# Kernel optimization log

Measured on AMD Instinct MI355X. Metric: run time of the kernel, lower is better.

## Reference

```python
import jax, jax.numpy as jnp
import numpy as np

N, E, C, H = 50000, 250000, 7, 64
D = C + 2  # node feature dim after concatenating labels


def _mlp2(x, w1, b1, w2, b2):
    return jnp.maximum(x @ w1 + b1, 0.0) @ w2 + b2


def _lin(key, fi, fo, bias=True):
    lim = 1.0 / np.sqrt(fi)
    kw, kb = jax.random.split(key)
    w = jax.random.uniform(kw, (fi, fo), jnp.float32, -lim, lim)
    if bias:
        b = jax.random.uniform(kb, (fo,), jnp.float32, -lim, lim)
        return w, b
    return w


def setup_inputs() -> dict:
    key = jax.random.key(0)
    ks = jax.random.split(key, 16)
    v = jax.random.normal(ks[0], (N, C), jnp.float32)
    labels = jnp.zeros((N, 2), jnp.float32).at[0, 1].set(1.0)  # node 0 is the goal
    edge_index = jax.random.randint(ks[1], (2, E), 0, N)
    hx_w1, hx_b1 = _lin(ks[2], 4 * D, H)
    hx_w2, hx_b2 = _lin(ks[3], H, H)
    hy_w1, hy_b1 = _lin(ks[4], 3 * D, H)
    hy_w2, hy_b2 = _lin(ks[5], H, H)
    fx_w1, fx_b1 = _lin(ks[6], 4 * H, H)
    fx_w2, fx_b2 = _lin(ks[7], H, H)
    fy_w1, fy_b1 = _lin(ks[8], 3 * H, H)
    fy_w2, fy_b2 = _lin(ks[9], H, H)
    feta_w1, feta_b1 = _lin(ks[10], H, H)
    feta_w2, feta_b2 = _lin(ks[11], H, H)
    feta_w3 = _lin(ks[12], H, 1, bias=False)
    return dict(v=v, labels=labels, edge_index=edge_index, loop=3,
                hx_w1=hx_w1, hx_b1=hx_b1, hx_w2=hx_w2, hx_b2=hx_b2,
                hy_w1=hy_w1, hy_b1=hy_b1, hy_w2=hy_w2, hy_b2=hy_b2,
                fx_w1=fx_w1, fx_b1=fx_b1, fx_w2=fx_w2, fx_b2=fx_b2,
                fy_w1=fy_w1, fy_b1=fy_b1, fy_w2=fy_w2, fy_b2=fy_b2,
                feta_w1=feta_w1, feta_b1=feta_b1, feta_w2=feta_w2, feta_b2=feta_b2,
                feta_w3=feta_w3)


def reference(v, labels, edge_index, loop,
              hx_w1, hx_b1, hx_w2, hx_b2,
              hy_w1, hy_b1, hy_w2, hy_b2,
              fx_w1, fx_b1, fx_w2, fx_b2,
              fy_w1, fy_b1, fy_w2, fy_b2,
              feta_w1, feta_b1, feta_w2, feta_b2, feta_w3):
    n = v.shape[0]
    vc = jnp.concatenate([v, labels], axis=-1)              # [N, D]
    goal = vc[jnp.argmax(labels[:, 1])][None, :]             # [1, D]
    d = vc - goal
    x = _mlp2(jnp.concatenate([vc, jnp.broadcast_to(goal, vc.shape), d, d * d], -1),
              hx_w1, hx_b1, hx_w2, hx_b2)                    # [N, H]
    src, dst = edge_index[0], edge_index[1]
    vi, vj = vc[src], vc[dst]
    y = _mlp2(jnp.concatenate([vj - vi, vj, vi], -1), hy_w1, hy_b1, hy_w2, hy_b2)  # [E, H]
    for _ in range(loop):
        # MPNN (PyG default flow): x_j = source = edge_index[0], x_i = target = edge_index[1]
        xj_m, xi_m = x[src], x[dst]
        m = _mlp2(jnp.concatenate([xj_m - xi_m, xj_m, xi_m, y], -1),
                  fx_w1, fx_b1, fx_w2, fx_b2)                # [E, H]
        agg = jax.ops.segment_max(m, dst, num_segments=n)    # scatter-max to targets; empty -> -inf
        x = jnp.maximum(x, agg)                              # -inf absorbed by max with x
        xi, xj = x[src], x[dst]                              # Explorer: i=edge_index[0], j=edge_index[1]
        y = jnp.maximum(y, _mlp2(jnp.concatenate([xj - xi, xj, xi], -1),
                                 fy_w1, fy_b1, fy_w2, fy_b2))
    h = jnp.maximum(x @ feta_w1 + feta_b1, 0.0)
    h = jnp.maximum(h @ feta_w2 + feta_b2, 0.0)
    return h @ feta_w3                                       # [N, 1]
```

## Files before the change

kernel.cpp:

```cpp
#include <hip/hip_runtime.h>
#include <math.h>

typedef unsigned short u16;
typedef unsigned int u32;
typedef unsigned long long u64;
typedef __attribute__((ext_vector_type(8))) _Float16 f16x8;
typedef __attribute__((ext_vector_type(2))) _Float16 f16x2;
typedef __attribute__((ext_vector_type(4))) float f32x4;

union U8h { f16x8 v; f16x2 p[4]; u32 u[4]; _Float16 s[8]; };
union U4h { _Float16 s[4]; u64 u; };

__device__ __forceinline__ void atomicMaxF(float* addr, float val) {
  if (val >= 0.0f) {
    atomicMax((int*)addr, __float_as_int(val));
  } else {
    atomicMin((unsigned int*)addr, (unsigned int)__float_as_int(val));
  }
}

__device__ __forceinline__ f16x2 pk(float a, float b) {
  return __builtin_bit_cast(f16x2, __builtin_amdgcn_cvt_pkrtz(a, b));
}

__device__ __forceinline__ void dec8h(const float* f, U8h& h, U8h& l) {
#pragma unroll
  for (int i = 0; i < 4; ++i) {
    float a = f[2 * i], b = f[2 * i + 1];
    f16x2 hp = pk(a, b);
    float ra = a - (float)hp[0];
    float rb = b - (float)hp[1];
    h.p[i] = hp;
    l.p[i] = pk(ra, rb);
  }
}

__device__ __forceinline__ void conv8_rne(const float* f, U8h& h) {
#pragma unroll
  for (int i = 0; i < 8; ++i) h.s[i] = (_Float16)f[i];
}

__device__ __forceinline__ void load_row(const float* p, float* f) {
  *(float4*)(f + 0)  = *(const float4*)(p);
  *(float4*)(f + 4)  = *(const float4*)(p + 4);
  *(float4*)(f + 8)  = *(const float4*)(p + 32);
  *(float4*)(f + 12) = *(const float4*)(p + 36);
}

struct RunCtx { bool chain1, chain2, chain3, suppress; };

__device__ __forceinline__ RunCtx run_ctx(const int dd[4], int lane, int q) {
  bool allsame = (dd[0] == dd[1]) && (dd[1] == dd[2]) && (dd[2] == dd[3]);
  int nfd1 = __shfl(dd[0], lane + 16, 64);
  int nfd2 = __shfl(dd[0], lane + 32, 64);
  int nfd3 = __shfl(dd[0], lane + 48, 64);
  int as = allsame ? 1 : 0;
  int nas1 = __shfl(as, lane + 16, 64);
  int nas2 = __shfl(as, lane + 32, 64);
  int pld = __shfl(dd[3], lane - 16, 64);
  RunCtx c;
  c.chain1 = (q < 3) && (nfd1 == dd[3]);
  c.chain2 = c.chain1 && (nas1 != 0) && (q < 2) && (nfd2 == dd[3]);
  c.chain3 = c.chain2 && (nas2 != 0) && (q < 1) && (nfd3 == dd[3]);
  c.suppress = (q > 0) && (pld == dd[0]);
  return c;
}

__device__ __forceinline__ void emit_t(const f32x4 o, const int dd[4], const RunCtx c,
                                       int lane, int m, int t, float* __restrict__ xnew) {
// ... 150 lines not shown
      for (int k = 0; k < 9; ++k) s += g[k] * hxw1[(9 + k) * 64 + c];
      b1p[c] = s;
    }
    return;
  }
  __shared__ int red[256];
  int s = 0;
  for (int i = threadIdx.x; i < 1024; i += 256) {
    int idx = b * 1024 + i;
    s += (idx < N) ? deg[idx] : 0;
  }
  red[threadIdx.x] = s; __syncthreads();
  for (int st = 128; st > 0; st >>= 1) {
    if (threadIdx.x < st) red[threadIdx.x] += red[threadIdx.x + st];
    __syncthreads();
  }
  if (threadIdx.x == 0) bsum[b] = red[0];
}

__global__ __launch_bounds__(256) void k_hx2s(
    const float* __restrict__ vcp, const float* __restrict__ goal,
    const _Float16* __restrict__ B1, const float* __restrict__ b1p,
    const _Float16* __restrict__ B2, const float* __restrict__ b2,
    float* __restrict__ xout, float* __restrict__ xout2, _Float16* __restrict__ xh, int N,
    const int* __restrict__ deg, const int* __restrict__ bsum, int* __restrict__ cursor, int NB) {
  if ((int)blockIdx.x >= NB) {
    __shared__ int lsum[256];
    __shared__ int bofs;
    int b = blockIdx.x - NB;
    int tid = threadIdx.x;
    if (tid == 0) {
      int a = 0;
      for (int i = 0; i < b; ++i) a += bsum[i];
      bofs = a;
    }
    int base_i = b * 1024 + tid * 4;
    int loc[4]; int s = 0;
#pragma unroll
    for (int j = 0; j < 4; ++j) {
      int vv = (base_i + j < N) ? deg[base_i + j] : 0;
      loc[j] = s; s += vv;
    }
    lsum[tid] = s; __syncthreads();
    for (int st = 1; st < 256; st <<= 1) {
      int add = (tid >= st) ? lsum[tid - st] : 0;
      __syncthreads();
      lsum[tid] += add;
      __syncthreads();
    }
    int toff = bofs + lsum[tid] - s;
#pragma unroll
    for (int j = 0; j < 4; ++j) {
      if (base_i + j < N) cursor[base_i + j] = toff + loc[j];
    }
    return;
  }
  __shared__ float hbuf[4][16 * 68];
  const int lane = threadIdx.x & 63;
  const int wv = threadIdx.x >> 6;
  const int m = lane & 15, q = lane >> 4;
  const int base = blockIdx.x * 64 + wv * 16;
  int node = base + m; if (node >= N) node = N - 1;
  float vc[12];
  *(float4*)(vc + 0) = *(const float4*)(vcp + (size_t)node * 16);
  *(float4*)(vc + 4) = *(const float4*)(vcp + (size_t)node * 16 + 4);
  *(float4*)(vc + 8) = *(const float4*)(vcp + (size_t)node * 16 + 8);
  float gl[9];
#pragma unroll
  for (int i = 0; i < 9; ++i) gl[i] = goal[i];
  float f[8];
#pragma unroll
  for (int j = 0; j < 8; ++j) {
    int idx = q * 8 + j;
    float val = 0.f;
    if (idx < 9) val = vc[idx];
    else if (idx < 18) val = vc[idx - 9] - gl[idx - 9];
    else if (idx < 27) { float dv = vc[idx - 18] - gl[idx - 18]; val = dv * dv; }
    f[j] = val;
  }
  U8h Ah, Al;
  dec8h(f, Ah, Al);

  f32x4 acc[4];
#pragma unroll
  for (int t = 0; t < 4; ++t) { float bv = b1p[t * 16 + m]; acc[t] = (f32x4){bv, bv, bv, bv}; }
#pragma unroll
  for (int t = 0; t < 4; ++t) {
    f16x8 b = *(const f16x8*)(B1 + ((size_t)t * 64 + lane) * 8);
    acc[t] = __builtin_amdgcn_mfma_f32_16x16x32_f16(Ah.v, b, acc[t], 0, 0, 0);
    acc[t] = __builtin_amdgcn_mfma_f32_16x16x32_f16(Al.v, b, acc[t], 0, 0, 0);
  }

  float* hb = hbuf[wv];
#pragma unroll
  for (int t = 0; t < 4; ++t)
#pragma unroll
    for (int r = 0; r < 4; ++r)
      hb[(q * 4 + r) * 68 + t * 16 + m] = fmaxf(acc[t][r], 0.f);

  float fh[16];
  load_row(hb + m * 68 + q * 8, fh);
  U8h A2h[2], A2l[2];
  dec8h(fh + 0, A2h[0], A2l[0]);
  dec8h(fh + 8, A2h[1], A2l[1]);

  f32x4 acc2[4];
#pragma unroll
  for (int t = 0; t < 4; ++t) { float bv = b2[t * 16 + m]; acc2[t] = (f32x4){bv, bv, bv, bv}; }
#pragma unroll
  for (int c = 0; c < 2; ++c) {
#pragma unroll
    for (int t = 0; t < 4; ++t) {
      f16x8 b = *(const f16x8*)(B2 + ((size_t)(c * 4 + t) * 64 + lane) * 8);
      acc2[t] = __builtin_amdgcn_mfma_f32_16x16x32_f16(A2h[c].v, b, acc2[t], 0, 0, 0);
      acc2[t] = __builtin_amdgcn_mfma_f32_16x16x32_f16(A2l[c].v, b, acc2[t], 0, 0, 0);
    }
  }

#pragma unroll
  for (int t = 0; t < 4; ++t)
#pragma unroll
    for (int r = 0; r < 4; ++r)
      hb[(q * 4 + r) * 68 + t * 16 + m] = acc2[t][r];

  int row = base + m;
  if (row < N) {
    float ov[16];
    const float* orow = hb + m * 68 + q * 16;
    *(float4*)(ov + 0)  = *(const float4*)(orow);
    *(float4*)(ov + 4)  = *(const float4*)(orow + 4);
    *(float4*)(ov + 8)  = *(const float4*)(orow + 8);
    *(float4*)(ov + 12) = *(const float4*)(orow + 12);
    float* p1 = xout + (size_t)row * 64 + q * 16;
    float* p2 = xout2 + (size_t)row * 64 + q * 16;
#pragma unroll
    for (int i = 0; i < 4; ++i) {
      *(float4*)(p1 + i * 4) = *(const float4*)(ov + i * 4);
      *(float4*)(p2 + i * 4) = *(const float4*)(ov + i * 4);
    }
    U8h X0, X1;
    conv8_rne(ov + 0, X0);
    conv8_rne(ov + 8, X1);
    *(f16x8*)(xh + (size_t)row * 64 + q * 16)     = X0.v;
    *(f16x8*)(xh + (size_t)row * 64 + q * 16 + 8) = X1.v;
  }
}

__global__ __launch_bounds__(256) void k_scatter(const int* __restrict__ src,
                                                 const int* __restrict__ dst, int E,
                                                 int* __restrict__ cursor,
                                                 int* __restrict__ srcp, int* __restrict__ dstp) {
  int e = blockIdx.x * 256 + threadIdx.x;
  if (e < E) {
    int d = dst[e];
    int pos = atomicAdd(&cursor[d], 1);
    srcp[pos] = src[e];
    dstp[pos] = d;
  }
}

__global__ __launch_bounds__(256) void k_cc(const float4* __restrict__ s,
                                            float4* __restrict__ d,
                                            _Float16* __restrict__ h16, int n4) {
  int i = blockIdx.x * 256 + threadIdx.x;
  if (i < n4) {
    float4 v = s[i];
    d[i] = v;
    U4h o;
    o.s[0] = (_Float16)v.x; o.s[1] = (_Float16)v.y;
    o.s[2] = (_Float16)v.z; o.s[3] = (_Float16)v.w;
    *(u64*)(h16 + (size_t)i * 4) = o.u;
  }
}

__global__ __launch_bounds__(256) void k_hyfx(
    const float* __restrict__ vcp, const _Float16* __restrict__ xh,
    const int* __restrict__ src, const int* __restrict__ dst,
    const _Float16* __restrict__ hB1, const float* __restrict__ hb1,
    const _Float16* __restrict__ hB2, const float* __restrict__ hb2,
    const _Float16* __restrict__ xB1, const float* __restrict__ xb1,
    const _Float16* __restrict__ xB2, const float* __restrict__ xb2,
    _Float16* __restrict__ y, float* __restrict__ xnew, int E) {
  __shared__ float hbuf[4][16 * 68];
  const int lane = threadIdx.x & 63;
  const int wv = threadIdx.x >> 6;
  const int m = lane & 15, q = lane >> 4;
  const int base = blockIdx.x * 64 + wv * 16;
  int em = base + m; if (em >= E) em = E - 1;
  const int si = src[em], di = dst[em];
  const int row = base + m;
  const bool live = row < E;

  int dd[4];
  int e0 = base + q * 4;
#pragma unroll
  for (int r = 0; r < 4; ++r) {
    int e2 = e0 + r;
    dd[r] = (e2 < E) ? dst[e2] : -1;
  }
  const int node = (q < 2) ? di : si;
  const float* p = vcp + (size_t)node * 16 + (q & 1) * 8;
  float f[8];
  *(float4*)(f + 0) = *(const float4*)(p);
  *(float4*)(f + 4) = *(const float4*)(p + 4);
  const _Float16* ps = xh + (size_t)si * 64 + q * 8;
  const _Float16* pd = xh + (size_t)di * 64 + q * 8;
  U8h Xs0, Xs1, Xd0, Xd1;
  Xs0.v = *(const f16x8*)ps;         Xs1.v = *(const f16x8*)(ps + 32);
  Xd0.v = *(const f16x8*)pd;         Xd1.v = *(const f16x8*)(pd + 32);

  U8h Ah, Al;
  dec8h(f, Ah, Al);

  f32x4 acc[4];
#pragma unroll
  for (int t = 0; t < 4; ++t) { float bv = hb1[t * 16 + m]; acc[t] = (f32x4){bv, bv, bv, bv}; }
#pragma unroll
  for (int t = 0; t < 4; ++t) {
    f16x8 b = *(const f16x8*)(hB1 + ((size_t)t * 64 + lane) * 8);
    acc[t] = __builtin_amdgcn_mfma_f32_16x16x32_f16(Ah.v, b, acc[t], 0, 0, 0);
    acc[t] = __builtin_amdgcn_mfma_f32_16x16x32_f16(Al.v, b, acc[t], 0, 0, 0);
  }

  float* hb = hbuf[wv];
#pragma unroll
  for (int t = 0; t < 4; ++t)
#pragma unroll
    for (int r = 0; r < 4; ++r)
      hb[(q * 4 + r) * 68 + t * 16 + m] = fmaxf(acc[t][r], 0.f);

  float fh[16];
  load_row(hb + m * 68 + q * 8, fh);
  U8h H0, H1;
  conv8_rne(fh + 0, H0);
  conv8_rne(fh + 8, H1);

  f32x4 o[4];
#pragma unroll
  for (int t = 0; t < 4; ++t) { float bv = hb2[t * 16 + m]; o[t] = (f32x4){bv, bv, bv, bv}; }
#pragma unroll
  for (int t = 0; t < 4; ++t) {
    f16x8 b0 = *(const f16x8*)(hB2 + ((size_t)(0 * 4 + t) * 64 + lane) * 8);
    f16x8 b1_ = *(const f16x8*)(hB2 + ((size_t)(1 * 4 + t) * 64 + lane) * 8);
    o[t] = __builtin_amdgcn_mfma_f32_16x16x32_f16(H0.v, b0, o[t], 0, 0, 0);
    o[t] = __builtin_amdgcn_mfma_f32_16x16x32_f16(H1.v, b1_, o[t], 0, 0, 0);
  }

#pragma unroll
  for (int t = 0; t < 4; ++t)
#pragma unroll
    for (int r = 0; r < 4; ++r)
      hb[(q * 4 + r) * 68 + t * 16 + m] = o[t][r];

  float nv[16];
  load_row(hb + m * 68 + q * 8, nv);
  U8h Yh0, Yh1;
  conv8_rne(nv + 0, Yh0);
  conv8_rne(nv + 8, Yh1);
  if (live) {
    size_t yo = (size_t)row * 64 + q * 8;
    *(f16x8*)(y + yo)      = Yh0.v;
    *(f16x8*)(y + yo + 32) = Yh1.v;
  }

  f32x4 acc2[4];
#pragma unroll
  for (int t = 0; t < 4; ++t) { float bv = xb1[t * 16 + m]; acc2[t] = (f32x4){bv, bv, bv, bv}; }
#pragma unroll
  for (int t = 0; t < 4; ++t) {
    f16x8 b0 = *(const f16x8*)(xB1 + ((size_t)(0 * 4 + t) * 64 + lane) * 8);
    f16x8 b1_ = *(const f16x8*)(xB1 + ((size_t)(1 * 4 + t) * 64 + lane) * 8);
    f16x8 b2_ = *(const f16x8*)(xB1 + ((size_t)(2 * 4 + t) * 64 + lane) * 8);
    f16x8 b3_ = *(const f16x8*)(xB1 + ((size_t)(3 * 4 + t) * 64 + lane) * 8);
    f16x8 b4_ = *(const f16x8*)(xB1 + ((size_t)(4 * 4 + t) * 64 + lane) * 8);
    f16x8 b5_ = *(const f16x8*)(xB1 + ((size_t)(5 * 4 + t) * 64 + lane) * 8);
    acc2[t] = __builtin_amdgcn_mfma_f32_16x16x32_f16(Xs0.v, b0, acc2[t], 0, 0, 0);
    acc2[t] = __builtin_amdgcn_mfma_f32_16x16x32_f16(Xs1.v, b1_, acc2[t], 0, 0, 0);
    acc2[t] = __builtin_amdgcn_mfma_f32_16x16x32_f16(Xd0.v, b2_, acc2[t], 0, 0, 0);
    acc2[t] = __builtin_amdgcn_mfma_f32_16x16x32_f16(Xd1.v, b3_, acc2[t], 0, 0, 0);
    acc2[t] = __builtin_amdgcn_mfma_f32_16x16x32_f16(Yh0.v, b4_, acc2[t], 0, 0, 0);
    acc2[t] = __builtin_amdgcn_mfma_f32_16x16x32_f16(Yh1.v, b5_, acc2[t], 0, 0, 0);
  }

#pragma unroll
  for (int t = 0; t < 4; ++t)
#pragma unroll
    for (int r = 0; r < 4; ++r)
      hb[(q * 4 + r) * 68 + t * 16 + m] = fmaxf(acc2[t][r], 0.f);

  float fh2[16];
  load_row(hb + m * 68 + q * 8, fh2);
  U8h G0, G1;
  conv8_rne(fh2 + 0, G0);
  conv8_rne(fh2 + 8, G1);

  f32x4 o2[4];
#pragma unroll
  for (int t = 0; t < 4; ++t) { float bv = xb2[t * 16 + m]; o2[t] = (f32x4){bv, bv, bv, bv}; }
#pragma unroll
  for (int t = 0; t < 4; ++t) {
    f16x8 b0 = *(const f16x8*)(xB2 + ((size_t)(0 * 4 + t) * 64 + lane) * 8);
    f16x8 b1_ = *(const f16x8*)(xB2 + ((size_t)(1 * 4 + t) * 64 + lane) * 8);
    o2[t] = __builtin_amdgcn_mfma_f32_16x16x32_f16(G0.v, b0, o2[t], 0, 0, 0);
    o2[t] = __builtin_amdgcn_mfma_f32_16x16x32_f16(G1.v, b1_, o2[t], 0, 0, 0);
  }

  RunCtx rc = run_ctx(dd, lane, q);
#pragma unroll
  for (int t = 0; t < 4; ++t) emit_t(o2[t], dd, rc, lane, m, t, xnew);
}

__global__ __launch_bounds__(256) void k_fyfx(
    const _Float16* __restrict__ xh, _Float16* __restrict__ y,
    const int* __restrict__ src, const int* __restrict__ dst,
    const _Float16* __restrict__ yB1, const float* __restrict__ yb1,
    const _Float16* __restrict__ yB2, const float* __restrict__ yb2,
    const _Float16* __restrict__ xB1, const float* __restrict__ xb1,
    const _Float16* __restrict__ xB2, const float* __restrict__ xb2,
    float* __restrict__ xnew, int E, int storeY) {
  __shared__ float hbuf[8][16 * 68];
  const int lane = threadIdx.x & 63;
  const int wv = threadIdx.x >> 6;
  const int m = lane & 15, q = lane >> 4;
  const int b0e = blockIdx.x * 128 + wv * 16;

  float* hb0 = hbuf[wv];
  float* hb1 = hbuf[4 + wv];

  int em0 = b0e + m;       if (em0 >= E) em0 = E - 1;
  int em1 = b0e + 64 + m;  if (em1 >= E) em1 = E - 1;
  const int si0 = src[em0], di0 = dst[em0];
  const int si1 = src[em1], di1 = dst[em1];
  const bool live0 = (b0e + m) < E;
  const bool live1 = (b0e + 64 + m) < E;

  U8h Xs0[2], Xs1[2], Xd0[2], Xd1[2], Ho0[2], Ho1[2];
  {
    const _Float16* ps = xh + (size_t)si0 * 64 + q * 8;
    const _Float16* pd = xh + (size_t)di0 * 64 + q * 8;
    Xs0[0].v = *(const f16x8*)ps;  Xs1[0].v = *(const f16x8*)(ps + 32);
    Xd0[0].v = *(const f16x8*)pd;  Xd1[0].v = *(const f16x8*)(pd + 32);
  }
  {
    const _Float16* ps = xh + (size_t)si1 * 64 + q * 8;
    const _Float16* pd = xh + (size_t)di1 * 64 + q * 8;
    Xs0[1].v = *(const f16x8*)ps;  Xs1[1].v = *(const f16x8*)(ps + 32);
    Xd0[1].v = *(const f16x8*)pd;  Xd1[1].v = *(const f16x8*)(pd + 32);
  }
  {
    size_t yo0 = (size_t)em0 * 64 + q * 8;
// ... 8 lines not shown
    float bv = yb1[t * 16 + m];
    acc[0][t] = (f32x4){bv, bv, bv, bv};
    acc[1][t] = acc[0][t];
  }
#pragma unroll
  for (int t = 0; t < 4; ++t) {
    f16x8 w0 = *(const f16x8*)(yB1 + ((size_t)(0 * 4 + t) * 64 + lane) * 8);
    f16x8 w1 = *(const f16x8*)(yB1 + ((size_t)(1 * 4 + t) * 64 + lane) * 8);
    f16x8 w2 = *(const f16x8*)(yB1 + ((size_t)(2 * 4 + t) * 64 + lane) * 8);
    f16x8 w3 = *(const f16x8*)(yB1 + ((size_t)(3 * 4 + t) * 64 + lane) * 8);
#pragma unroll
    for (int u = 0; u < 2; ++u) {
      acc[u][t] = __builtin_amdgcn_mfma_f32_16x16x32_f16(Xd0[u].v, w0, acc[u][t], 0, 0, 0);
      acc[u][t] = __builtin_amdgcn_mfma_f32_16x16x32_f16(Xd1[u].v, w1, acc[u][t], 0, 0, 0);
      acc[u][t] = __builtin_amdgcn_mfma_f32_16x16x32_f16(Xs0[u].v, w2, acc[u][t], 0, 0, 0);
      acc[u][t] = __builtin_amdgcn_mfma_f32_16x16x32_f16(Xs1[u].v, w3, acc[u][t], 0, 0, 0);
    }
  }

#pragma unroll
  for (int t = 0; t < 4; ++t)
#pragma unroll
    for (int r = 0; r < 4; ++r) {
      hb0[(q * 4 + r) * 68 + t * 16 + m] = fmaxf(acc[0][t][r], 0.f);
      hb1[(q * 4 + r) * 68 + t * 16 + m] = fmaxf(acc[1][t][r], 0.f);
    }

  float fh0[16], fh1[16];
  load_row(hb0 + m * 68 + q * 8, fh0);
  load_row(hb1 + m * 68 + q * 8, fh1);
  U8h H0[2], H1[2];
  conv8_rne(fh0 + 0, H0[0]); conv8_rne(fh0 + 8, H1[0]);
  conv8_rne(fh1 + 0, H0[1]); conv8_rne(fh1 + 8, H1[1]);

  f32x4 o[2][4];
#pragma unroll
  for (int t = 0; t < 4; ++t) {
    float bv = yb2[t * 16 + m];
    o[0][t] = (f32x4){bv, bv, bv, bv};
    o[1][t] = o[0][t];
  }
#pragma unroll
  for (int t = 0; t < 4; ++t) {
    f16x8 w0 = *(const f16x8*)(yB2 + ((size_t)(0 * 4 + t) * 64 + lane) * 8);
    f16x8 w1 = *(const f16x8*)(yB2 + ((size_t)(1 * 4 + t) * 64 + lane) * 8);
#pragma unroll
    for (int u = 0; u < 2; ++u) {
      o[u][t] = __builtin_amdgcn_mfma_f32_16x16x32_f16(H0[u].v, w0, o[u][t], 0, 0, 0);
      o[u][t] = __builtin_amdgcn_mfma_f32_16x16x32_f16(H1[u].v, w1, o[u][t], 0, 0, 0);
    }
  }

#pragma unroll
  for (int t = 0; t < 4; ++t)
#pragma unroll
    for (int r = 0; r < 4; ++r) {
      hb0[(q * 4 + r) * 68 + t * 16 + m] = o[0][t][r];
      hb1[(q * 4 + r) * 68 + t * 16 + m] = o[1][t][r];
    }

  float nv0[16], nv1[16];
  load_row(hb0 + m * 68 + q * 8, nv0);
  load_row(hb1 + m * 68 + q * 8, nv1);
#pragma unroll
  for (int i = 0; i < 8; ++i) {
    nv0[i]     = fmaxf((float)Ho0[0].s[i], nv0[i]);
    nv0[8 + i] = fmaxf((float)Ho1[0].s[i], nv0[8 + i]);
    nv1[i]     = fmaxf((float)Ho0[1].s[i], nv1[i]);
    nv1[8 + i] = fmaxf((float)Ho1[1].s[i], nv1[8 + i]);
  }
  U8h Yh0[2], Yh1[2];
  conv8_rne(nv0 + 0, Yh0[0]); conv8_rne(nv0 + 8, Yh1[0]);
  conv8_rne(nv1 + 0, Yh0[1]); conv8_rne(nv1 + 8, Yh1[1]);
  if (storeY) {
    if (live0) {
      size_t yo = (size_t)(b0e + m) * 64 + q * 8;
      *(f16x8*)(y + yo)      = Yh0[0].v;
      *(f16x8*)(y + yo + 32) = Yh1[0].v;
    }
    if (live1) {
      size_t yo = (size_t)(b0e + 64 + m) * 64 + q * 8;
      *(f16x8*)(y + yo)      = Yh0[1].v;
      *(f16x8*)(y + yo + 32) = Yh1[1].v;
    }
  }

// ... 7 lines not shown
#pragma unroll
  for (int t = 0; t < 4; ++t) {
    f16x8 w0 = *(const f16x8*)(xB1 + ((size_t)(0 * 4 + t) * 64 + lane) * 8);
    f16x8 w1 = *(const f16x8*)(xB1 + ((size_t)(1 * 4 + t) * 64 + lane) * 8);
    f16x8 w2 = *(const f16x8*)(xB1 + ((size_t)(2 * 4 + t) * 64 + lane) * 8);
    f16x8 w3 = *(const f16x8*)(xB1 + ((size_t)(3 * 4 + t) * 64 + lane) * 8);
    f16x8 w4 = *(const f16x8*)(xB1 + ((size_t)(4 * 4 + t) * 64 + lane) * 8);
    f16x8 w5 = *(const f16x8*)(xB1 + ((size_t)(5 * 4 + t) * 64 + lane) * 8);
#pragma unroll
    for (int u = 0; u < 2; ++u) {
      acc2[u][t] = __builtin_amdgcn_mfma_f32_16x16x32_f16(Xs0[u].v, w0, acc2[u][t], 0, 0, 0);
      acc2[u][t] = __builtin_amdgcn_mfma_f32_16x16x32_f16(Xs1[u].v, w1, acc2[u][t], 0, 0, 0);
      acc2[u][t] = __builtin_amdgcn_mfma_f32_16x16x32_f16(Xd0[u].v, w2, acc2[u][t], 0, 0, 0);
      acc2[u][t] = __builtin_amdgcn_mfma_f32_16x16x32_f16(Xd1[u].v, w3, acc2[u][t], 0, 0, 0);
      acc2[u][t] = __builtin_amdgcn_mfma_f32_16x16x32_f16(Yh0[u].v, w4, acc2[u][t], 0, 0, 0);
      acc2[u][t] = __builtin_amdgcn_mfma_f32_16x16x32_f16(Yh1[u].v, w5, acc2[u][t], 0, 0, 0);
    }
  }

#pragma unroll
  for (int t = 0; t < 4; ++t)
#pragma unroll
    for (int r = 0; r < 4; ++r) {
      hb0[(q * 4 + r) * 68 + t * 16 + m] = fmaxf(acc2[0][t][r], 0.f);
      hb1[(q * 4 + r) * 68 + t * 16 + m] = fmaxf(acc2[1][t][r], 0.f);
    }

  float g0v[16], g1v[16];
  load_row(hb0 + m * 68 + q * 8, g0v);
  load_row(hb1 + m * 68 + q * 8, g1v);
  U8h G0[2], G1[2];
  conv8_rne(g0v + 0, G0[0]); conv8_rne(g0v + 8, G1[0]);
  conv8_rne(g1v + 0, G0[1]); conv8_rne(g1v + 8, G1[1]);

  int dd0[4], dd1[4];
  {
    int e0 = b0e + q * 4;
#pragma unroll
    for (int r = 0; r < 4; ++r) {
      int e2 = e0 + r;
      dd0[r] = (e2 < E) ? dst[e2] : -1;
      int e3 = e2 + 64;
      dd1[r] = (e3 < E) ? dst[e3] : -1;
    }
  }

  f32x4 o2[2][4];
#pragma unroll
  for (int t = 0; t < 4; ++t) {
    float bv = xb2[t * 16 + m];
    o2[0][t] = (f32x4){bv, bv, bv, bv};
    o2[1][t] = o2[0][t];
  }
// ... 1 lines not shown
  for (int t = 0; t < 4; ++t) {
    f16x8 w0 = *(const f16x8*)(xB2 + ((size_t)(0 * 4 + t) * 64 + lane) * 8);
    f16x8 w1 = *(const f16x8*)(xB2 + ((size_t)(1 * 4 + t) * 64 + lane) * 8);
#pragma unroll
    for (int u = 0; u < 2; ++u) {
      o2[u][t] = __builtin_amdgcn_mfma_f32_16x16x32_f16(G0[u].v, w0, o2[u][t], 0, 0, 0);
      o2[u][t] = __builtin_amdgcn_mfma_f32_16x16x32_f16(G1[u].v, w1, o2[u][t], 0, 0, 0);
    }
  }

  RunCtx rc0 = run_ctx(dd0, lane, q);
#pragma unroll
  for (int t = 0; t < 4; ++t) emit_t(o2[0][t], dd0, rc0, lane, m, t, xnew);
  RunCtx rc1 = run_ctx(dd1, lane, q);
#pragma unroll
  for (int t = 0; t < 4; ++t) emit_t(o2[1][t], dd1, rc1, lane, m, t, xnew);
}

__global__ __launch_bounds__(256) void k_feta2(
    const float* __restrict__ x,
    const _Float16* __restrict__ B1, const float* __restrict__ b1,
    const _Float16* __restrict__ B2, const float* __restrict__ b2,
    const float* __restrict__ w3, float* __restrict__ out, int N) {
  __shared__ float hbuf[4][16 * 68];
  const int lane = threadIdx.x & 63;
  const int wv = threadIdx.x >> 6;
  const int m = lane & 15, q = lane >> 4;
  const int base = blockIdx.x * 64 + wv * 16;
  int node = base + m; if (node >= N) node = N - 1;
  float fs[16];
  load_row(x + (size_t)node * 64 + q * 8, fs);
  U8h Ah[2], Al[2];
  dec8h(fs + 0, Ah[0], Al[0]);
  dec8h(fs + 8, Ah[1], Al[1]);

  f32x4 acc[4];
#pragma unroll
  for (int t = 0; t < 4; ++t) { float bv = b1[t * 16 + m]; acc[t] = (f32x4){bv, bv, bv, bv}; }
#pragma unroll
  for (int c = 0; c < 2; ++c) {
#pragma unroll
    for (int t = 0; t < 4; ++t) {
      f16x8 b = *(const f16x8*)(B1 + ((size_t)(c * 4 + t) * 64 + lane) * 8);
      acc[t] = __builtin_amdgcn_mfma_f32_16x16x32_f16(Ah[c].v, b, acc[t], 0, 0, 0);
      acc[t] = __builtin_amdgcn_mfma_f32_16x16x32_f16(Al[c].v, b, acc[t], 0, 0, 0);
    }
  }

  float* hb = hbuf[wv];
#pragma unroll
  for (int t = 0; t < 4; ++t)
#pragma unroll
    for (int r = 0; r < 4; ++r)
      hb[(q * 4 + r) * 68 + t * 16 + m] = fmaxf(acc[t][r], 0.f);

  float fh[16];
  load_row(hb + m * 68 + q * 8, fh);
  U8h A2h[2], A2l[2];
  dec8h(fh + 0, A2h[0], A2l[0]);
  dec8h(fh + 8, A2h[1], A2l[1]);

  f32x4 acc2[4];
#pragma unroll
  for (int t = 0; t < 4; ++t) { float bv = b2[t * 16 + m]; acc2[t] = (f32x4){bv, bv, bv, bv}; }
#pragma unroll
  for (int c = 0; c < 2; ++c) {
#pragma unroll
    for (int t = 0; t < 4; ++t) {
      f16x8 b = *(const f16x8*)(B2 + ((size_t)(c * 4 + t) * 64 + lane) * 8);
      acc2[t] = __builtin_amdgcn_mfma_f32_16x16x32_f16(A2h[c].v, b, acc2[t], 0, 0, 0);
      acc2[t] = __builtin_amdgcn_mfma_f32_16x16x32_f16(A2l[c].v, b, acc2[t], 0, 0, 0);
    }
  }

  float w3v[4];
#pragma unroll
  for (int t = 0; t < 4; ++t) w3v[t] = w3[t * 16 + m];
#pragma unroll
  for (int r = 0; r < 4; ++r) {
    float s = 0.f;
// ... 25 lines not shown
  const float* fx_w1 = (const float*)d_in[12];
  const float* fx_b1 = (const float*)d_in[13];
  const float* fx_w2 = (const float*)d_in[14];
  const float* fx_b2 = (const float*)d_in[15];
  const float* fy_w1 = (const float*)d_in[16];
  const float* fy_b1 = (const float*)d_in[17];
  const float* fy_w2 = (const float*)d_in[18];
  const float* fy_b2 = (const float*)d_in[19];
  const float* feta_w1 = (const float*)d_in[20];
  const float* feta_b1 = (const float*)d_in[21];
  const float* feta_w2 = (const float*)d_in[22];
  const float* feta_b2 = (const float*)d_in[23];
  const float* feta_w3 = (const float*)d_in[24];

  int N = in_sizes[0] / 7;
  int E = in_sizes[2] / 2;
  const int* src = ei;
  const int* dst = ei + E;

  char* wsb = (char*)d_ws;
  float* goal = (float*)wsb;
  u64* goalkey = (u64*)(wsb + 64);
  float* b1p = (float*)(wsb + 96);
  float* xa = (float*)(wsb + 512);
  float* xb = xa + (size_t)N * 64;
  _Float16* xh = (_Float16*)(xb + (size_t)N * 64);
  _Float16* y = xh + (size_t)N * 64;
  _Float16* wp = y + (size_t)E * 64;
  float* vcp = (float*)(wp + 49152);
  int* deg = (int*)(vcp + (size_t)N * 16);
  int* cursor = deg + N;
  int* srcp = cursor + N;
  int* dstp = srcp + E;
  int* bsum = dstp + E;

  _Float16* fxB1 = wp;          _Float16* fxB2 = wp + 12288;
  _Float16* fyB1 = wp + 16384;  _Float16* fyB2 = wp + 24576;
  _Float16* hyB1 = wp + 28672;  _Float16* hyB2 = wp + 30720;
  _Float16* hxB1 = wp + 34816;  _Float16* hxB2 = wp + 36864;
  _Float16* feB1 = wp + 40960;  _Float16* feB2 = wp + 45056;

  int SB = (N + 1023) / 1024;
  int NB = (N + 63) / 64;
  int EB = (E + 63) / 64;
  int EB2 = (E + 127) / 128;

  k_prep<<<25, 256, 0, stream>>>(fx_w1, fx_w2, fy_w1, fy_w2, hy_w1, hy_w2,
                                 hx_w1, hx_w2, feta_w1, feta_w2, wp, goalkey, deg, N);
  k_vch<<<(N * 16 + 255) / 256, 256, 0, stream>>>(v, labels, vcp, N, dst, E, deg, goalkey);
  k_scan1g<<<SB + 1, 256, 0, stream>>>(deg, N, SB, bsum, v, labels, goalkey,
                                       hx_w1, hx_b1, goal, b1p);
  k_hx2s<<<NB + SB, 256, 0, stream>>>(vcp, goal, hxB1, b1p, hxB2, hx_b2, xa, xb, xh, N,
                                      deg, bsum, cursor, NB);
  k_scatter<<<(E + 255) / 256, 256, 0, stream>>>(src, dst, E, cursor, srcp, dstp);

  k_hyfx<<<EB, 256, 0, stream>>>(vcp, xh, srcp, dstp,
                                 hyB1, hy_b1, hyB2, hy_b2,
                                 fxB1, fx_b1, fxB2, fx_b2, y, xb, E);
  k_cc<<<(N * 16 + 255) / 256, 256, 0, stream>>>((const float4*)xb, (float4*)xa, xh, N * 16);
  k_fyfx<<<EB2, 256, 0, stream>>>(xh, y, srcp, dstp,
                                  fyB1, fy_b1, fyB2, fy_b2,
                                  fxB1, fx_b1, fxB2, fx_b2, xa, E, 1);
  k_cc<<<(N * 16 + 255) / 256, 256, 0, stream>>>((const float4*)xa, (float4*)xb, xh, N * 16);
  k_fyfx<<<EB2, 256, 0, stream>>>(xh, y, srcp, dstp,
                                  fyB1, fy_b1, fyB2, fy_b2,
                                  fxB1, fx_b1, fxB2, fx_b2, xb, E, 0);

  k_feta2<<<NB, 256, 0, stream>>>(xb, feB1, feta_b1, feB2, feta_b2, feta_w3,
                                  (float*)d_out, N);
}
```

Measured before the change: 326.2 us.

## Use single in-place x buffer, swizzled LDS staging, and two-tile hyfx

```diff
diff --git a/kernel.cpp b/kernel.cpp
--- a/kernel.cpp
+++ b/kernel.cpp
@@ -45,6 +45,27 @@
   *(float4*)(f + 4)  = *(const float4*)(p + 4);
   *(float4*)(f + 8)  = *(const float4*)(p + 32);
   *(float4*)(f + 12) = *(const float4*)(p + 36);
+}
+
+__device__ __forceinline__ int swz(int row, int col) {
+  return (row << 6) + (col ^ ((row & 7) << 2));
+}
+
+__device__ __forceinline__ void load_row_swz(const float* hb, int m, int q, float* f) {
+  int s = (m & 7) << 2;
+  const float* r = hb + (m << 6);
+  *(float4*)(f + 0)  = *(const float4*)(r + ((q * 8)      ^ s));
+  *(float4*)(f + 4)  = *(const float4*)(r + ((q * 8 + 4)  ^ s));
+  *(float4*)(f + 8)  = *(const float4*)(r + ((q * 8 + 32) ^ s));
+  *(float4*)(f + 12) = *(const float4*)(r + ((q * 8 + 36) ^ s));
+}
+
+__device__ __forceinline__ void load_16_swz(const float* hb, int m, int c0, float* f) {
+  int s = (m & 7) << 2;
+  const float* r = hb + (m << 6);
+#pragma unroll
+  for (int j = 0; j < 4; ++j)
+    *(float4*)(f + 4 * j) = *(const float4*)(r + ((c0 + 4 * j) ^ s));
 }
 
 struct RunCtx { bool chain1, chain2, chain3, suppress; };
@@ -241,7 +262,7 @@
     const float* __restrict__ vcp, const float* __restrict__ goal,
     const _Float16* __restrict__ B1, const float* __restrict__ b1p,
     const _Float16* __restrict__ B2, const float* __restrict__ b2,
-    float* __restrict__ xout, float* __restrict__ xout2, _Float16* __restrict__ xh, int N,
+    float* __restrict__ xout, _Float16* __restrict__ xh, int N,
     const int* __restrict__ deg, const int* __restrict__ bsum, int* __restrict__ cursor, int NB) {
   if ((int)blockIdx.x >= NB) {
     __shared__ int lsum[256];
@@ -274,7 +295,7 @@
     }
     return;
   }
-  __shared__ float hbuf[4][16 * 68];
+  __shared__ float hbuf[4][16 * 64];
   const int lane = threadIdx.x & 63;
   const int wv = threadIdx.x >> 6;
   const int m = lane & 15, q = lane >> 4;
@@ -315,10 +336,10 @@
   for (int t = 0; t < 4; ++t)
 #pragma unroll
     for (int r = 0; r < 4; ++r)
-      hb[(q * 4 + r) * 68 + t * 16 + m] = fmaxf(acc[t][r], 0.f);
+      hb[swz(q * 4 + r, t * 16 + m)] = fmaxf(acc[t][r], 0.f);
 
   float fh[16];
-  load_row(hb + m * 68 + q * 8, fh);
+  load_row_swz(hb, m, q, fh);
   U8h A2h[2], A2l[2];
   dec8h(fh + 0, A2h[0], A2l[0]);
   dec8h(fh + 8, A2h[1], A2l[1]);
@@ -340,22 +361,16 @@
   for (int t = 0; t < 4; ++t)
 #pragma unroll
     for (int r = 0; r < 4; ++r)
-      hb[(q * 4 + r) * 68 + t * 16 + m] = acc2[t][r];
+      hb[swz(q * 4 + r, t * 16 + m)] = acc2[t][r];
 
   int row = base + m;
   if (row < N) {
     float ov[16];
-    const float* orow = hb + m * 68 + q * 16;
-    *(float4*)(ov + 0)  = *(const float4*)(orow);
-    *(float4*)(ov + 4)  = *(const float4*)(orow + 4);
-    *(float4*)(ov + 8)  = *(const float4*)(orow + 8);
-    *(float4*)(ov + 12) = *(const float4*)(orow + 12);
+    load_16_swz(hb, m, q * 16, ov);
     float* p1 = xout + (size_t)row * 64 + q * 16;
-    float* p2 = xout2 + (size_t)row * 64 + q * 16;
 #pragma unroll
     for (int i = 0; i < 4; ++i) {
       *(float4*)(p1 + i * 4) = *(const float4*)(ov + i * 4);
-      *(float4*)(p2 + i * 4) = *(const float4*)(ov + i * 4);
     }
     U8h X0, X1;
     conv8_rne(ov + 0, X0);
@@ -378,13 +393,11 @@
   }
 }
 
-__global__ __launch_bounds__(256) void k_cc(const float4* __restrict__ s,
-                                            float4* __restrict__ d,
+__global__ __launch_bounds__(256) void k_ch(const float4* __restrict__ s,
                                             _Float16* __restrict__ h16, int n4) {
   int i = blockIdx.x * 256 + threadIdx.x;
   if (i < n4) {
     float4 v = s[i];
-    d[i] = v;
     U4h o;
     o.s[0] = (_Float16)v.x; o.s[1] = (_Float16)v.y;
     o.s[2] = (_Float16)v.z; o.s[3] = (_Float16)v.w;
@@ -400,133 +413,205 @@
     const _Float16* __restrict__ xB1, const float* __restrict__ xb1,
     const _Float16* __restrict__ xB2, const float* __restrict__ xb2,
     _Float16* __restrict__ y, float* __restrict__ xnew, int E) {
-  __shared__ float hbuf[4][16 * 68];
+  __shared__ float hbuf[8][16 * 64];
   const int lane = threadIdx.x & 63;
   const int wv = threadIdx.x >> 6;
   const int m = lane & 15, q = lane >> 4;
-  const int base = blockIdx.x * 64 + wv * 16;
-  int em = base + m; if (em >= E) em = E - 1;
-  const int si = src[em], di = dst[em];
-  const int row = base + m;
-  const bool live = row < E;
-
-  int dd[4];
-  int e0 = base + q * 4;
-#pragma unroll
-  for (int r = 0; r < 4; ++r) {
-    int e2 = e0 + r;
-    dd[r] = (e2 < E) ? dst[e2] : -1;
-  }
-  const int node = (q < 2) ? di : si;
-  const float* p = vcp + (size_t)node * 16 + (q & 1) * 8;
-  float f[8];
-  *(float4*)(f + 0) = *(const float4*)(p);
-  *(float4*)(f + 4) = *(const float4*)(p + 4);
-  const _Float16* ps = xh + (size_t)si * 64 + q * 8;
-  const _Float16* pd = xh + (size_t)di * 64 + q * 8;
-  U8h Xs0, Xs1, Xd0, Xd1;
-  Xs0.v = *(const f16x8*)ps;         Xs1.v = *(const f16x8*)(ps + 32);
-  Xd0.v = *(const f16x8*)pd;         Xd1.v = *(const f16x8*)(pd + 32);
-
-  U8h Ah, Al;
-  dec8h(f, Ah, Al);
-
-  f32x4 acc[4];
-#pragma unroll
-  for (int t = 0; t < 4; ++t) { float bv = hb1[t * 16 + m]; acc[t] = (f32x4){bv, bv, bv, bv}; }
-#pragma unroll
-  for (int t = 0; t < 4; ++t) {
-    f16x8 b = *(const f16x8*)(hB1 + ((size_t)t * 64 + lane) * 8);
-    acc[t] = __builtin_amdgcn_mfma_f32_16x16x32_f16(Ah.v, b, acc[t], 0, 0, 0);
-    acc[t] = __builtin_amdgcn_mfma_f32_16x16x32_f16(Al.v, b, acc[t], 0, 0, 0);
-  }
-
-  float* hb = hbuf[wv];
+  const int b0e = blockIdx.x * 128 + wv * 16;
+  float* hb0 = hbuf[wv];
+  float* hbx = hbuf[4 + wv];
+
+  int em0 = b0e + m;       if (em0 >= E) em0 = E - 1;
+  int em1 = b0e + 64 + m;  if (em1 >= E) em1 = E - 1;
+  const int si0 = src[em0], di0 = dst[em0];
+  const int si1 = src[em1], di1 = dst[em1];
+  const bool live0 = (b0e + m) < E;
+  const bool live1 = (b0e + 64 + m) < E;
+
+  U8h Xs0[2], Xs1[2], Xd0[2], Xd1[2];
+  {
+    const _Float16* ps = xh + (size_t)si0 * 64 + q * 8;
+    const _Float16* pd = xh + (size_t)di0 * 64 + q * 8;
+    Xs0[0].v = *(const f16x8*)ps;  Xs1[0].v = *(const f16x8*)(ps + 32);
+    Xd0[0].v = *(const f16x8*)pd;  Xd1[0].v = *(const f16x8*)(pd + 32);
+  }
+  {
+    const _Float16* ps = xh + (size_t)si1 * 64 + q * 8;
+    const _Float16* pd = xh + (size_t)di1 * 64 + q * 8;
+    Xs0[1].v = *(const f16x8*)ps;  Xs1[1].v = *(const f16x8*)(ps + 32);
+    Xd0[1].v = *(const f16x8*)pd;  Xd1[1].v = *(const f16x8*)(pd + 32);
+  }
+
+  U8h Ah[2], Al[2];
+  {
+    const int n0 = (q < 2) ? di0 : si0;
+    const float* p = vcp + (size_t)n0 * 16 + (q & 1) * 8;
+    float f[8];
+    *(float4*)(f + 0) = *(const float4*)(p);
+    *(float4*)(f + 4) = *(const float4*)(p + 4);
+    dec8h(f, Ah[0], Al[0]);
+  }
+  {
+    const int n1 = (q < 2) ? di1 : si1;
+    const float* p = vcp + (size_t)n1 * 16 + (q & 1) * 8;
+    float f[8];
+    *(float4*)(f + 0) = *(const float4*)(p);
+    *(float4*)(f + 4) = *(const float4*)(p + 4);
+    dec8h(f, Ah[1], Al[1]);
+  }
+
+  f32x4 acc[2][4];
+#pragma unroll
+  for (int t = 0; t < 4; ++t) {
+    float bv = hb1[t * 16 + m];
+    acc[0][t] = (f32x4){bv, bv, bv, bv};
+    acc[1][t] = acc[0][t];
+  }
+#pragma unroll
+  for (int t = 0; t < 4; ++t) {
+    f16x8 w = *(const f16x8*)(hB1 + ((size_t)t * 64 + lane) * 8);
+#pragma unroll
+    for (int u = 0; u < 2; ++u) {
+      acc[u][t] = __builtin_amdgcn_mfma_f32_16x16x32_f16(Ah[u].v, w, acc[u][t], 0, 0, 0);
+      acc[u][t] = __builtin_amdgcn_mfma_f32_16x16x32_f16(Al[u].v, w, acc[u][t], 0, 0, 0);
+    }
+  }
+
 #pragma unroll
   for (int t = 0; t < 4; ++t)
 #pragma unroll
-    for (int r = 0; r < 4; ++r)
-      hb[(q * 4 + r) * 68 + t * 16 + m] = fmaxf(acc[t][r], 0.f);
-
-  float fh[16];
-  load_row(hb + m * 68 + q * 8, fh);
-  U8h H0, H1;
-  conv8_rne(fh + 0, H0);
-  conv8_rne(fh + 8, H1);
-
-  f32x4 o[4];
-#pragma unroll
-  for (int t = 0; t < 4; ++t) { float bv = hb2[t * 16 + m]; o[t] = (f32x4){bv, bv, bv, bv}; }
-#pragma unroll
-  for (int t = 0; t < 4; ++t) {
-    f16x8 b0 = *(const f16x8*)(hB2 + ((size_t)(0 * 4 + t) * 64 + lane) * 8);
-    f16x8 b1_ = *(const f16x8*)(hB2 + ((size_t)(1 * 4 + t) * 64 + lane) * 8);
-    o[t] = __builtin_amdgcn_mfma_f32_16x16x32_f16(H0.v, b0, o[t], 0, 0, 0);
-    o[t] = __builtin_amdgcn_mfma_f32_16x16x32_f16(H1.v, b1_, o[t], 0, 0, 0);
+    for (int r = 0; r < 4; ++r) {
+      hb0[swz(q * 4 + r, t * 16 + m)] = fmaxf(acc[0][t][r], 0.f);
+      hbx[swz(q * 4 + r, t * 16 + m)] = fmaxf(acc[1][t][r], 0.f);
+    }
+
+  float fh0[16], fh1[16];
+  load_row_swz(hb0, m, q, fh0);
+  load_row_swz(hbx, m, q, fh1);
+  U8h H0[2], H1[2];
+  conv8_rne(fh0 + 0, H0[0]); conv8_rne(fh0 + 8, H1[0]);
+  conv8_rne(fh1 + 0, H0[1]); conv8_rne(fh1 + 8, H1[1]);
+
+  f32x4 o[2][4];
+#pragma unroll
+  for (int t = 0; t < 4; ++t) {
+    float bv = hb2[t * 16 + m];
+    o[0][t] = (f32x4){bv, bv, bv, bv};
+    o[1][t] = o[0][t];
+  }
+#pragma unroll
+  for (int t = 0; t < 4; ++t) {
+    f16x8 w0 = *(const f16x8*)(hB2 + ((size_t)(0 * 4 + t) * 64 + lane) * 8);
+    f16x8 w1 = *(const f16x8*)(hB2 + ((size_t)(1 * 4 + t) * 64 + lane) * 8);
+#pragma unroll
+    for (int u = 0; u < 2; ++u) {
+      o[u][t] = __builtin_amdgcn_mfma_f32_16x16x32_f16(H0[u].v, w0, o[u][t], 0, 0, 0);
+      o[u][t] = __builtin_amdgcn_mfma_f32_16x16x32_f16(H1[u].v, w1, o[u][t], 0, 0, 0);
+    }
   }
 
 #pragma unroll
   for (int t = 0; t < 4; ++t)
 #pragma unroll
-    for (int r = 0; r < 4; ++r)
-      hb[(q * 4 + r) * 68 + t * 16 + m] = o[t][r];
-
-  float nv[16];
-  load_row(hb + m * 68 + q * 8, nv);
-  U8h Yh0, Yh1;
-  conv8_rne(nv + 0, Yh0);
-  conv8_rne(nv + 8, Yh1);
-  if (live) {
-    size_t yo = (size_t)row * 64 + q * 8;
-    *(f16x8*)(y + yo)      = Yh0.v;
-    *(f16x8*)(y + yo + 32) = Yh1.v;
-  }
-
-  f32x4 acc2[4];
-#pragma unroll
-  for (int t = 0; t < 4; ++t) { float bv = xb1[t * 16 + m]; acc2[t] = (f32x4){bv, bv, bv, bv}; }
-#pragma unroll
-  for (int t = 0; t < 4; ++t) {
-    f16x8 b0 = *(const f16x8*)(xB1 + ((size_t)(0 * 4 + t) * 64 + lane) * 8);
-    f16x8 b1_ = *(const f16x8*)(xB1 + ((size_t)(1 * 4 + t) * 64 + lane) * 8);
-    f16x8 b2_ = *(const f16x8*)(xB1 + ((size_t)(2 * 4 + t) * 64 + lane) * 8);
-    f16x8 b3_ = *(const f16x8*)(xB1 + ((size_t)(3 * 4 + t) * 64 + lane) * 8);
-    f16x8 b4_ = *(const f16x8*)(xB1 + ((size_t)(4 * 4 + t) * 64 + lane) * 8);
-    f16x8 b5_ = *(const f16x8*)(xB1 + ((size_t)(5 * 4 + t) * 64 + lane) * 8);
-    acc2[t] = __builtin_amdgcn_mfma_f32_16x16x32_f16(Xs0.v, b0, acc2[t], 0, 0, 0);
-    acc2[t] = __builtin_amdgcn_mfma_f32_16x16x32_f16(Xs1.v, b1_, acc2[t], 0, 0, 0);
-    acc2[t] = __builtin_amdgcn_mfma_f32_16x16x32_f16(Xd0.v, b2_, acc2[t], 0, 0, 0);
-    acc2[t] = __builtin_amdgcn_mfma_f32_16x16x32_f16(Xd1.v, b3_, acc2[t], 0, 0, 0);
-    acc2[t] = __builtin_amdgcn_mfma_f32_16x16x32_f16(Yh0.v, b4_, acc2[t], 0, 0, 0);
-    acc2[t] = __builtin_amdgcn_mfma_f32_16x16x32_f16(Yh1.v, b5_, acc2[t], 0, 0, 0);
+    for (int r = 0; r < 4; ++r) {
+      hb0[swz(q * 4 + r, t * 16 + m)] = o[0][t][r];
+      hbx[swz(q * 4 + r, t * 16 + m)] = o[1][t][r];
+    }
+
+  float nv0[16], nv1[16];
+  load_row_swz(hb0, m, q, nv0);
+  load_row_swz(hbx, m, q, nv1);
+  U8h Yh0[2], Yh1[2];
+  conv8_rne(nv0 + 0, Yh0[0]); conv8_rne(nv0 + 8, Yh1[0]);
+  conv8_rne(nv1 + 0, Yh0[1]); conv8_rne(nv1 + 8, Yh1[1]);
+  if (live0) {
+    size_t yo = (size_t)(b0e + m) * 64 + q * 8;
+    *(f16x8*)(y + yo)      = Yh0[0].v;
+    *(f16x8*)(y + yo + 32) = Yh1[0].v;
+  }
+  if (live1) {
+    size_t yo = (size_t)(b0e + 64 + m) * 64 + q * 8;
+    *(f16x8*)(y + yo)      = Yh0[1].v;
+    *(f16x8*)(y + yo + 32) = Yh1[1].v;
+  }
+
+  f32x4 acc2[2][4];
+#pragma unroll
+  for (int t = 0; t < 4; ++t) {
+    float bv = xb1[t * 16 + m];
+    acc2[0][t] = (f32x4){bv, bv, bv, bv};
+    acc2[1][t] = acc2[0][t];
+  }
+#pragma unroll
+  for (int t = 0; t < 4; ++t) {
+    f16x8 w0 = *(const f16x8*)(xB1 + ((size_t)(0 * 4 + t) * 64 + lane) * 8);
+    f16x8 w1 = *(const f16x8*)(xB1 + ((size_t)(1 * 4 + t) * 64 + lane) * 8);
+    f16x8 w2 = *(const f16x8*)(xB1 + ((size_t)(2 * 4 + t) * 64 + lane) * 8);
+    f16x8 w3 = *(const f16x8*)(xB1 + ((size_t)(3 * 4 + t) * 64 + lane) * 8);
+    f16x8 w4 = *(const f16x8*)(xB1 + ((size_t)(4 * 4 + t) * 64 + lane) * 8);
+    f16x8 w5 = *(const f16x8*)(xB1 + ((size_t)(5 * 4 + t) * 64 + lane) * 8);
+#pragma unroll
+    for (int u = 0; u < 2; ++u) {
+      acc2[u][t] = __builtin_amdgcn_mfma_f32_16x16x32_f16(Xs0[u].v, w0, acc2[u][t], 0, 0, 0);
+      acc2[u][t] = __builtin_amdgcn_mfma_f32_16x16x32_f16(Xs1[u].v, w1, acc2[u][t], 0, 0, 0);
+      acc2[u][t] = __builtin_amdgcn_mfma_f32_16x16x32_f16(Xd0[u].v, w2, acc2[u][t], 0, 0, 0);
+      acc2[u][t] = __builtin_amdgcn_mfma_f32_16x16x32_f16(Xd1[u].v, w3, acc2[u][t], 0, 0, 0);
+      acc2[u][t] = __builtin_amdgcn_mfma_f32_16x16x32_f16(Yh0[u].v, w4, acc2[u][t], 0, 0, 0);
+      acc2[u][t] = __builtin_amdgcn_mfma_f32_16x16x32_f16(Yh1[u].v, w5, acc2[u][t], 0, 0, 0);
+    }
   }
 
 #pragma unroll
   for (int t = 0; t < 4; ++t)
 #pragma unroll
-    for (int r = 0; r < 4; ++r)
-      hb[(q * 4 + r) * 68 + t * 16 + m] = fmaxf(acc2[t][r], 0.f);
-
-  float fh2[16];
-  load_row(hb + m * 68 + q * 8, fh2);
-  U8h G0, G1;
-  conv8_rne(fh2 + 0, G0);
-  conv8_rne(fh2 + 8, G1);
-
-  f32x4 o2[4];
-#pragma unroll
-  for (int t = 0; t < 4; ++t) { float bv = xb2[t * 16 + m]; o2[t] = (f32x4){bv, bv, bv, bv}; }
-#pragma unroll
-  for (int t = 0; t < 4; ++t) {
-    f16x8 b0 = *(const f16x8*)(xB2 + ((size_t)(0 * 4 + t) * 64 + lane) * 8);
-    f16x8 b1_ = *(const f16x8*)(xB2 + ((size_t)(1 * 4 + t) * 64 + lane) * 8);
-    o2[t] = __builtin_amdgcn_mfma_f32_16x16x32_f16(G0.v, b0, o2[t], 0, 0, 0);
-    o2[t] = __builtin_amdgcn_mfma_f32_16x16x32_f16(G1.v, b1_, o2[t], 0, 0, 0);
-  }
-
-  RunCtx rc = run_ctx(dd, lane, q);
-#pragma unroll
-  for (int t = 0; t < 4; ++t) emit_t(o2[t], dd, rc, lane, m, t, xnew);
+    for (int r = 0; r < 4; ++r) {
+      hb0[swz(q * 4 + r, t * 16 + m)] = fmaxf(acc2[0][t][r], 0.f);
+      hbx[swz(q * 4 + r, t * 16 + m)] = fmaxf(acc2[1][t][r], 0.f);
+    }
+
+  float g0v[16], g1v[16];
+  load_row_swz(hb0, m, q, g0v);
+  load_row_swz(hbx, m, q, g1v);
+  U8h G0[2], G1[2];
+  conv8_rne(g0v + 0, G0[0]); conv8_rne(g0v + 8, G1[0]);
+  conv8_rne(g1v + 0, G0[1]); conv8_rne(g1v + 8, G1[1]);
+
+  int dd0[4], dd1[4];
+  {
+    int e0 = b0e + q * 4;
+#pragma unroll
+    for (int r = 0; r < 4; ++r) {
+      int e2 = e0 + r;
+      dd0[r] = (e2 < E) ? dst[e2] : -1;
+      int e3 = e2 + 64;
+      dd1[r] = (e3 < E) ? dst[e3] : -1;
+    }
+  }
+
+  f32x4 o2[2][4];
+#pragma unroll
+  for (int t = 0; t < 4; ++t) {
+    float bv = xb2[t * 16 + m];
+    o2[0][t] = (f32x4){bv, bv, bv, bv};
+    o2[1][t] = o2[0][t];
+  }
+#pragma unroll
+  for (int t = 0; t < 4; ++t) {
+    f16x8 w0 = *(const f16x8*)(xB2 + ((size_t)(0 * 4 + t) * 64 + lane) * 8);
+    f16x8 w1 = *(const f16x8*)(xB2 + ((size_t)(1 * 4 + t) * 64 + lane) * 8);
+#pragma unroll
+    for (int u = 0; u < 2; ++u) {
+      o2[u][t] = __builtin_amdgcn_mfma_f32_16x16x32_f16(G0[u].v, w0, o2[u][t], 0, 0, 0);
+      o2[u][t] = __builtin_amdgcn_mfma_f32_16x16x32_f16(G1[u].v, w1, o2[u][t], 0, 0, 0);
+    }
+  }
+
+  RunCtx rc0 = run_ctx(dd0, lane, q);
+#pragma unroll
+  for (int t = 0; t < 4; ++t) emit_t(o2[0][t], dd0, rc0, lane, m, t, xnew);
+  RunCtx rc1 = run_ctx(dd1, lane, q);
+#pragma unroll
+  for (int t = 0; t < 4; ++t) emit_t(o2[1][t], dd1, rc1, lane, m, t, xnew);
 }
 
 __global__ __launch_bounds__(256) void k_fyfx(
@@ -537,14 +622,13 @@
     const _Float16* __restrict__ xB1, const float* __restrict__ xb1,
     const _Float16* __restrict__ xB2, const float* __restrict__ xb2,
     float* __restrict__ xnew, int E, int storeY) {
-  __shared__ float hbuf[8][16 * 68];
+  __shared__ float hbuf[8][16 * 64];
   const int lane = threadIdx.x & 63;
   const int wv = threadIdx.x >> 6;
   const int m = lane & 15, q = lane >> 4;
   const int b0e = blockIdx.x * 128 + wv * 16;
-
   float* hb0 = hbuf[wv];
-  float* hb1 = hbuf[4 + wv];
+  float* hbx = hbuf[4 + wv];
 
   int em0 = b0e + m;       if (em0 >= E) em0 = E - 1;
   int em1 = b0e + 64 + m;  if (em1 >= E) em1 = E - 1;
@@ -599,13 +683,13 @@
   for (int t = 0; t < 4; ++t)
 #pragma unroll
     for (int r = 0; r < 4; ++r) {
-      hb0[(q * 4 + r) * 68 + t * 16 + m] = fmaxf(acc[0][t][r], 0.f);
-      hb1[(q * 4 + r) * 68 + t * 16 + m] = fmaxf(acc[1][t][r], 0.f);
+      hb0[swz(q * 4 + r, t * 16 + m)] = fmaxf(acc[0][t][r], 0.f);
+      hbx[swz(q * 4 + r, t * 16 + m)] = fmaxf(acc[1][t][r], 0.f);
     }
 
   float fh0[16], fh1[16];
-  load_row(hb0 + m * 68 + q * 8, fh0);
-  load_row(hb1 + m * 68 + q * 8, fh1);
+  load_row_swz(hb0, m, q, fh0);
+  load_row_swz(hbx, m, q, fh1);
   U8h H0[2], H1[2];
   conv8_rne(fh0 + 0, H0[0]); conv8_rne(fh0 + 8, H1[0]);
   conv8_rne(fh1 + 0, H0[1]); conv8_rne(fh1 + 8, H1[1]);
@@ -632,13 +716,13 @@
   for (int t = 0; t < 4; ++t)
 #pragma unroll
     for (int r = 0; r < 4; ++r) {
-      hb0[(q * 4 + r) * 68 + t * 16 + m] = o[0][t][r];
-      hb1[(q * 4 + r) * 68 + t * 16 + m] = o[1][t][r];
+      hb0[swz(q * 4 + r, t * 16 + m)] = o[0][t][r];
+      hbx[swz(q * 4 + r, t * 16 + m)] = o[1][t][r];
     }
 
   float nv0[16], nv1[16];
-  load_row(hb0 + m * 68 + q * 8, nv0);
-  load_row(hb1 + m * 68 + q * 8, nv1);
+  load_row_swz(hb0, m, q, nv0);
+  load_row_swz(hbx, m, q, nv1);
 #pragma unroll
   for (int i = 0; i < 8; ++i) {
     nv0[i]     = fmaxf((float)Ho0[0].s[i], nv0[i]);
@@ -692,13 +776,13 @@
   for (int t = 0; t < 4; ++t)
 #pragma unroll
     for (int r = 0; r < 4; ++r) {
-      hb0[(q * 4 + r) * 68 + t * 16 + m] = fmaxf(acc2[0][t][r], 0.f);
-      hb1[(q * 4 + r) * 68 + t * 16 + m] = fmaxf(acc2[1][t][r], 0.f);
+      hb0[swz(q * 4 + r, t * 16 + m)] = fmaxf(acc2[0][t][r], 0.f);
+      hbx[swz(q * 4 + r, t * 16 + m)] = fmaxf(acc2[1][t][r], 0.f);
     }
 
   float g0v[16], g1v[16];
-  load_row(hb0 + m * 68 + q * 8, g0v);
-  load_row(hb1 + m * 68 + q * 8, g1v);
+  load_row_swz(hb0, m, q, g0v);
+  load_row_swz(hbx, m, q, g1v);
   U8h G0[2], G1[2];
   conv8_rne(g0v + 0, G0[0]); conv8_rne(g0v + 8, G1[0]);
   conv8_rne(g1v + 0, G0[1]); conv8_rne(g1v + 8, G1[1]);
@@ -746,7 +830,7 @@
     const _Float16* __restrict__ B1, const float* __restrict__ b1,
     const _Float16* __restrict__ B2, const float* __restrict__ b2,
     const float* __restrict__ w3, float* __restrict__ out, int N) {
-  __shared__ float hbuf[4][16 * 68];
+  __shared__ float hbuf[4][16 * 64];
   const int lane = threadIdx.x & 63;
   const int wv = threadIdx.x >> 6;
   const int m = lane & 15, q = lane >> 4;
@@ -776,10 +860,10 @@
   for (int t = 0; t < 4; ++t)
 #pragma unroll
     for (int r = 0; r < 4; ++r)
-      hb[(q * 4 + r) * 68 + t * 16 + m] = fmaxf(acc[t][r], 0.f);
+      hb[swz(q * 4 + r, t * 16 + m)] = fmaxf(acc[t][r], 0.f);
 
   float fh[16];
-  load_row(hb + m * 68 + q * 8, fh);
+  load_row_swz(hb, m, q, fh);
   U8h A2h[2], A2l[2];
   dec8h(fh + 0, A2h[0], A2l[0]);
   dec8h(fh + 8, A2h[1], A2l[1]);
@@ -851,9 +935,8 @@
   float* goal = (float*)wsb;
   u64* goalkey = (u64*)(wsb + 64);
   float* b1p = (float*)(wsb + 96);
-  float* xa = (float*)(wsb + 512);
-  float* xb = xa + (size_t)N * 64;
-  _Float16* xh = (_Float16*)(xb + (size_t)N * 64);
+  float* x = (float*)(wsb + 512);
+  _Float16* xh = (_Float16*)(x + (size_t)N * 64);
   _Float16* y = xh + (size_t)N * 64;
   _Float16* wp = y + (size_t)E * 64;
   float* vcp = (float*)(wp + 49152);
@@ -871,7 +954,6 @@
 
   int SB = (N + 1023) / 1024;
   int NB = (N + 63) / 64;
-  int EB = (E + 63) / 64;
   int EB2 = (E + 127) / 128;
 
   k_prep<<<25, 256, 0, stream>>>(fx_w1, fx_w2, fy_w1, fy_w2, hy_w1, hy_w2,
@@ -879,22 +961,22 @@
   k_vch<<<(N * 16 + 255) / 256, 256, 0, stream>>>(v, labels, vcp, N, dst, E, deg, goalkey);
   k_scan1g<<<SB + 1, 256, 0, stream>>>(deg, N, SB, bsum, v, labels, goalkey,
                                        hx_w1, hx_b1, goal, b1p);
-  k_hx2s<<<NB + SB, 256, 0, stream>>>(vcp, goal, hxB1, b1p, hxB2, hx_b2, xa, xb, xh, N,
+  k_hx2s<<<NB + SB, 256, 0, stream>>>(vcp, goal, hxB1, b1p, hxB2, hx_b2, x, xh, N,
                                       deg, bsum, cursor, NB);
   k_scatter<<<(E + 255) / 256, 256, 0, stream>>>(src, dst, E, cursor, srcp, dstp);
 
-  k_hyfx<<<EB, 256, 0, stream>>>(vcp, xh, srcp, dstp,
-                                 hyB1, hy_b1, hyB2, hy_b2,
-                                 fxB1, fx_b1, fxB2, fx_b2, y, xb, E);
-  k_cc<<<(N * 16 + 255) / 256, 256, 0, stream>>>((const float4*)xb, (float4*)xa, xh, N * 16);
+  k_hyfx<<<EB2, 256, 0, stream>>>(vcp, xh, srcp, dstp,
+                                  hyB1, hy_b1, hyB2, hy_b2,
+                                  fxB1, fx_b1, fxB2, fx_b2, y, x, E);
+  k_ch<<<(N * 16 + 255) / 256, 256, 0, stream>>>((const float4*)x, xh, N * 16);
   k_fyfx<<<EB2, 256, 0, stream>>>(xh, y, srcp, dstp,
                                   fyB1, fy_b1, fyB2, fy_b2,
-                                  fxB1, fx_b1, fxB2, fx_b2, xa, E, 1);
-  k_cc<<<(N * 16 + 255) / 256, 256, 0, stream>>>((const float4*)xa, (float4*)xb, xh, N * 16);
+                                  fxB1, fx_b1, fxB2, fx_b2, x, E, 1);
+  k_ch<<<(N * 16 + 255) / 256, 256, 0, stream>>>((const float4*)x, xh, N * 16);
   k_fyfx<<<EB2, 256, 0, stream>>>(xh, y, srcp, dstp,
                                   fyB1, fy_b1, fyB2, fy_b2,
-                                  fxB1, fx_b1, fxB2, fx_b2, xb, E, 0);
-
-  k_feta2<<<NB, 256, 0, stream>>>(xb, feB1, feta_b1, feB2, feta_b2, feta_w3,
+                                  fxB1, fx_b1, fxB2, fx_b2, x, E, 0);
+
+  k_feta2<<<NB, 256, 0, stream>>>(x, feB1, feta_b1, feB2, feta_b2, feta_w3,
                                   (float*)d_out, N);
 }
```

After: 333.2 us. 1.02x slower.
